# Kernel optimization log

Measured on AMD Instinct MI355X. Metric: run time of the kernel, lower is better.

Reference implementation:

```python
import jax, jax.numpy as jnp
import numpy as np

NUM_GROUP = 16
LN_EPS = 1e-5


def setup_inputs() -> dict:
    key = jax.random.key(0)
    ks = jax.random.split(key, 3)
    B, N, C = 8, 4096, 1024
    x = jax.random.normal(ks[0], (B, N, C), dtype=jnp.float32)
    Wqkv = jax.random.normal(ks[1], (C, 3 * C), dtype=jnp.float32) * (C ** -0.5)
    Wproj = jax.random.normal(ks[2], (C, C), dtype=jnp.float32) * (C ** -0.5)
    bproj = jnp.zeros((C,), dtype=jnp.float32)
    gamma = jnp.ones((C,), dtype=jnp.float32)
    beta = jnp.zeros((C,), dtype=jnp.float32)
    return {"x": x, "Wqkv": Wqkv, "Wproj": Wproj, "bproj": bproj,
            "gamma": gamma, "beta": beta}


def reference(x, Wqkv, Wproj, bproj, gamma, beta):
    B, N, C = x.shape
    G = NUM_GROUP
    hd = C // G
    scale = hd ** -0.5
    # QKV projection: [B,N,3,G,hd]
    qkv = (x @ Wqkv).reshape(B, N, 3, G, hd)
    q = jnp.transpose(qkv[:, :, 0], (0, 2, 1, 3))  # [B,G,N,hd]
    k = jnp.transpose(qkv[:, :, 1], (0, 2, 1, 3)) * scale
    v = jnp.transpose(qkv[:, :, 2], (0, 2, 1, 3))
    # transposed (channel) attention: k^T @ v -> [B,G,hd,hd]
    attn = jnp.einsum('bgnd,bgne->bgde', k, v)
    attn = jax.nn.softmax(attn, axis=-1)
    # (attn @ q^T)^T : out[b,g,n,d] = sum_e attn[b,g,d,e] * q[b,g,n,e]
    out = jnp.einsum('bgde,bgne->bgnd', attn, q)  # [B,G,N,hd]
    out = jnp.transpose(out, (0, 2, 1, 3)).reshape(B, N, C)
    out = out @ Wproj + bproj  # dropout is identity in eval mode
    h = x + out
    # LayerNorm over last dim
    mu = jnp.mean(h, axis=-1, keepdims=True)
    var = jnp.var(h, axis=-1, keepdims=True)
    return gamma * (h - mu) * jax.lax.rsqrt(var + LN_EPS) + beta
```

## Files before the change

### kernel.cpp

```cpp
#include <hip/hip_runtime.h>
#include <cstdint>

typedef __bf16 bf16;
typedef __bf16 bf16x8 __attribute__((ext_vector_type(8)));
typedef float f32x4 __attribute__((ext_vector_type(4)));

#define DEVI __device__ __forceinline__

DEVI float bits2f(uint32_t u){ union{uint32_t u;float f;}x; x.u=u; return x.f; }
DEVI uint32_t packbf2(float a, float b){
  union{ bf16 h[2]; uint32_t u; } p; p.h[0]=(bf16)a; p.h[1]=(bf16)b; return p.u;
}

DEVI void gload_lds16(const void* g, void* l){
  __builtin_amdgcn_global_load_lds(
    (const __attribute__((address_space(1))) uint32_t*)g,
    (__attribute__((address_space(3))) uint32_t*)l, 16, 0, 0);
}

__global__ __launch_bounds__(256) void k_cast(const float* __restrict__ x, bf16* __restrict__ o, int n){
  int i = (blockIdx.x*256 + threadIdx.x)*8;
  if (i >= n) return;
  float4 a = *(const float4*)(x+i);
  float4 b = *(const float4*)(x+i+4);
  union { bf16 h[8]; uint4 u; } r;
  r.h[0]=(bf16)a.x; r.h[1]=(bf16)a.y; r.h[2]=(bf16)a.z; r.h[3]=(bf16)a.w;
  r.h[4]=(bf16)b.x; r.h[5]=(bf16)b.y; r.h[6]=(bf16)b.z; r.h[7]=(bf16)b.w;
  *(uint4*)(o+i) = r.u;
}

__global__ __launch_bounds__(256) void k_castT(const float* __restrict__ x, bf16* __restrict__ xb,
                                               bf16* __restrict__ xT){
  const int b = blockIdx.z;
  x  += (size_t)b*4194304; xb += (size_t)b*4194304; xT += (size_t)b*4194304;
  const int n0 = blockIdx.y*64, c0 = blockIdx.x*64;
  __shared__ float sF[64][65];
  const int t = threadIdx.x;
  const int lr = t>>4, lc4 = (t&15)*4;
  #pragma unroll
  for (int i=0;i<4;++i){
    int r = lr + i*16;
    float4 v = *(const float4*)(x + (size_t)(n0+r)*1024 + c0 + lc4);
    sF[r][lc4+0]=v.x; sF[r][lc4+1]=v.y; sF[r][lc4+2]=v.z; sF[r][lc4+3]=v.w;
  }
  __syncthreads();
  const int wr = t>>3, wc8 = (t&7)*8;
  #pragma unroll
  for (int i=0;i<2;++i){
    int r = wr + i*32;
    union{ bf16 h[8]; uint4 u; } p;
    #pragma unroll
    for (int j=0;j<8;++j) p.h[j] = (bf16)sF[r][wc8+j];
    *(uint4*)(xb + (size_t)(n0+r)*1024 + c0 + wc8) = p.u;
  }
  #pragma unroll
  for (int i=0;i<2;++i){
    int c = wr + i*32;
    union{ bf16 h[8]; uint4 u; } p;
    #pragma unroll
    for (int j=0;j<8;++j) p.h[j] = (bf16)sF[wc8+j][c];
    *(uint4*)(xT + (size_t)(c0+c)*4096 + n0 + wc8) = p.u;
  }
}

__global__ __launch_bounds__(256) void k_transpose(const float* __restrict__ W, bf16* __restrict__ WT,
                                                   int R, int Ccols){
  __shared__ float tile[32][33];
  int bc = blockIdx.x*32, br = blockIdx.y*32;
  int lc = threadIdx.x & 31, lr = threadIdx.x >> 5;
  #pragma unroll
  for (int i=0;i<4;i++){
    int r = lr + i*8;
    tile[r][lc] = W[(size_t)(br+r)*Ccols + bc + lc];
  }
  __syncthreads();
  #pragma unroll
  for (int i=0;i<4;i++){
    int r = lr + i*8;
    WT[(size_t)(bc+r)*R + br + lc] = (bf16)tile[lc][r];
  }
}

__global__ __launch_bounds__(256) void k_gemm128(
    const bf16* __restrict__ A, const bf16* __restrict__ BT, bf16* __restrict__ C,
    int N, int K, int lda, int ldb,
    size_t As, size_t Bs, size_t Cs)
{
  A += blockIdx.z*As; BT += blockIdx.z*Bs; C += blockIdx.z*Cs;
  __shared__ __align__(16) bf16 sA[128*64];
  __shared__ __align__(16) bf16 sB[128*64];
  const int t = threadIdx.x, w = t>>6, l = t&63;
  const int bm = blockIdx.y*128, bn = blockIdx.x*128;
  const int wr = (w>>1)*64, wc = (w&1)*64;
  f32x4 acc[4][4] = {};
  const int srow = l>>3;
  const int scol = ((l&7) ^ (l>>3))*8;
  const int nk = K>>6;
  for (int kt=0; kt<nk; ++kt) {
    const int k0 = kt*64;
    #pragma unroll
    for (int i=0;i<4;++i){
      int c = w*4+i;
      int row = c*8 + srow;
      gload_lds16(A  + (size_t)(bm+row)*lda + k0 + scol, (char*)sA + c*1024);
      gload_lds16(BT + (size_t)(bn+row)*ldb + k0 + scol, (char*)sB + c*1024);
    }
    __syncthreads();
    #pragma unroll
    for (int kk=0; kk<64; kk+=32) {
      bf16x8 af[4], bfr[4];
      const int xr = ((kk + 8*(l>>4))*2) ^ ((l&7)<<4);
      #pragma unroll
      for (int mf=0;mf<4;++mf){
        int row = wr + mf*16 + (l&15);
        af[mf] = *(const bf16x8*)((const char*)sA + row*128 + xr);
      }
      #pragma unroll
      for (int nf=0;nf<4;++nf){
        int row = wc + nf*16 + (l&15);
        bfr[nf] = *(const bf16x8*)((const char*)sB + row*128 + xr);
      }
      #pragma unroll
      for (int mf=0;mf<4;++mf)
        #pragma unroll
        for (int nf=0;nf<4;++nf)
          acc[mf][nf] = __builtin_amdgcn_mfma_f32_16x16x32_bf16(af[mf], bfr[nf], acc[mf][nf], 0,0,0);
    }
    __syncthreads();
  }
  #pragma unroll
  for (int mf=0;mf<4;++mf)
    #pragma unroll
    for (int nf=0;nf<4;++nf)
      #pragma unroll
      for (int r=0;r<4;++r){
        int row = bm + wr + mf*16 + (l>>4)*4 + r;
        int col = bn + wc + nf*16 + (l&15);
        C[(size_t)row*N + col] = (bf16)acc[mf][nf][r];
      }
}

__global__ __launch_bounds__(256) void k_gramsym(const bf16* __restrict__ xT, bf16* __restrict__ Gram){
  const int d = blockIdx.y*36 + blockIdx.x;
  const int vt = (d & 7)*36 + (d >> 3);
  const int b = vt/36;
  int t36 = vt - b*36;
  int i = 0;
  while (t36 >= 8 - i){ t36 -= 8 - i; ++i; }
  const int j = i + t36;
  const bf16* A = xT + (size_t)b*4194304;
  bf16* C = Gram + (size_t)b*1048576;
  const int bm = i*128, bn = j*128;

  __shared__ __align__(16) bf16 sAB[16384];
  bf16* sA = sAB; bf16* sB = sAB + 8192;
  const int t = threadIdx.x, w = t>>6, l = t&63;
  const int wr = (w>>1)*64, wc = (w&1)*64;
  f32x4 acc[4][4] = {};
  const int srow = l>>3;
  const int scol = ((l&7) ^ (l>>3))*8;
  for (int kt=0; kt<64; ++kt) {
    const int k0 = kt*64;
    #pragma unroll
    for (int ii=0;ii<4;++ii){
      int c = w*4+ii;
      int row = c*8 + srow;
      gload_lds16(A + (size_t)(bm+row)*4096 + k0 + scol, (char*)sA + c*1024);
      gload_lds16(A + (size_t)(bn+row)*4096 + k0 + scol, (char*)sB + c*1024);
    }
    __syncthreads();
    #pragma unroll
    for (int kk=0; kk<64; kk+=32) {
      bf16x8 af[4], bfr[4];
      const int xr = ((kk + 8*(l>>4))*2) ^ ((l&7)<<4);
      #pragma unroll
      for (int mf=0;mf<4;++mf)
        af[mf] = *(const bf16x8*)((const char*)sA + (wr+mf*16+(l&15))*128 + xr);
      #pragma unroll
      for (int nf=0;nf<4;++nf)
        bfr[nf] = *(const bf16x8*)((const char*)sB + (wc+nf*16+(l&15))*128 + xr);
      #pragma unroll
      for (int mf=0;mf<4;++mf)
        #pragma unroll
        for (int nf=0;nf<4;++nf)
          acc[mf][nf] = __builtin_amdgcn_mfma_f32_16x16x32_bf16(af[mf], bfr[nf], acc[mf][nf], 0,0,0);
    }
    __syncthreads();
  }
  #pragma unroll
  for (int mf=0;mf<4;++mf)
    #pragma unroll
    for (int nf=0;nf<4;++nf)
      #pragma unroll
      for (int r=0;r<4;++r){
        int row = bm + wr + mf*16 + (l>>4)*4 + r;
        int col = bn + wc + nf*16 + (l&15);
        C[(size_t)row*1024 + col] = (bf16)acc[mf][nf][r];
      }
  if (i == j) return;
  for (int h2=0; h2<2; ++h2){
    __syncthreads();
    if ((w&1) == h2){
      #pragma unroll
      for (int mf=0;mf<4;++mf)
        #pragma unroll
        for (int nf=0;nf<4;++nf)
          #pragma unroll
          for (int p=0;p<2;++p){
            int col_local = nf*16 + (l&15);
            int rowb = wr + mf*16 + (l>>4)*4 + 2*p;
            *(uint32_t*)((char*)sAB + (col_local*136 + rowb)*2) =
              packbf2(acc[mf][nf][2*p], acc[mf][nf][2*p+1]);
          }
    }
    __syncthreads();
    {
      int col_local = t>>2, sub = t&3;
      const uint4* src = (const uint4*)((const char*)sAB + col_local*272 + sub*64);
      uint4 v0 = src[0], v1 = src[1], v2 = src[2], v3 = src[3];
      bf16* dst = C + (size_t)(bn + h2*64 + col_local)*1024 + bm + sub*32;
      ((uint4*)dst)[0]=v0; ((uint4*)dst)[1]=v1; ((uint4*)dst)[2]=v2; ((uint4*)dst)[3]=v3;
    }
  }
}

__global__ __launch_bounds__(512, 2) void k_gemm256(
    const bf16* __restrict__ A, const bf16* __restrict__ BT, bf16* __restrict__ C,
    int N, int K,
    const float* __restrict__ bias, const bf16* __restrict__ resid,
    size_t As, size_t Bs, size_t Cs, size_t Rs)
{
  A += blockIdx.z*As; BT += blockIdx.z*Bs; C += blockIdx.z*Cs; resid += blockIdx.z*Rs;
  __shared__ __align__(16) bf16 lds[2][2][256*64];
  bf16* bA0 = &lds[0][0][0]; bf16* bB0 = &lds[0][1][0];
  bf16* bA1 = &lds[1][0][0]; bf16* bB1 = &lds[1][1][0];

  const int t = threadIdx.x, w = t>>6, l = t&63;
  const int wm = w>>2, wn = w&3;

  const int nwg = gridDim.x * gridDim.y;
  const int orig = blockIdx.y * gridDim.x + blockIdx.x;
  const int q = nwg >> 3, r = nwg & 7;
  const int xcd = orig & 7, loc = orig >> 3;
  const int swz = (xcd < r ? xcd*(q+1) : r*(q+1) + (xcd-r)*q) + loc;
  const int bx = swz % gridDim.x, by = swz / gridDim.x;
  const int bm = by*256, bn = bx*256;

  const int co0 = (16*(l>>4)) ^ ((l&7)<<4);
  const int co1 = (64 + 16*(l>>4)) ^ ((l&7)<<4);

  auto stageA = [&](const bf16* G, bf16* Ldst, int j, int k0){
    int row = wm*128 + wn*32 + j*8 + (l>>3);
    int col = 8*((l&7) ^ (l>>3));
    gload_lds16(G + (size_t)(bm + row)*K + k0 + col,
                Ldst + (wm*128 + wn*32 + j*8)*64);
  };
  auto stageB = [&](const bf16* G, bf16* Ldst, int j, int k0){
    int row = j*64 + w*8 + (l>>3);
    int col = 8*((l&7) ^ (l>>3));
    gload_lds16(G + (size_t)(bn + row)*K + k0 + col,
                Ldst + (j*64 + w*8)*64);
  };

#define RD_AA(dst, qd, base) {                                                  \
    const int r0 = wm*128 + (qd)*32 + (l&15);                                   \
    dst[0][0] = *(const bf16x8*)((const char*)(base) + (r0   )*128 + co0);      \
    dst[0][1] = *(const bf16x8*)((const char*)(base) + (r0   )*128 + co1);      \
    dst[1][0] = *(const bf16x8*)((const char*)(base) + (r0+16)*128 + co0);      \
    dst[1][1] = *(const bf16x8*)((const char*)(base) + (r0+16)*128 + co1);      \
  }

#define MFMA_Q(P, AA) {                                                         \
    __builtin_amdgcn_s_setprio(1);                                              \
    _Pragma("unroll")                                                           \
    for (int kk=0;kk<2;++kk)                                                    \
      _Pragma("unroll")                                                         \
      for (int i=0;i<2;++i)                                                     \
        _Pragma("unroll")                                                       \
        for (int nf=0;nf<4;++nf)                                                \
          acc[2*(P)+i][nf] = __builtin_amdgcn_mfma_f32_16x16x32_bf16(           \
              AA[i][kk], bfr[nf][kk], acc[2*(P)+i][nf], 0,0,0);                 \
    __builtin_amdgcn_s_setprio(0);                                              \
  }

#define BAR asm volatile("s_barrier" ::: "memory")

  f32x4 acc[8][4] = {};
  const int NT = K >> 6;

  #pragma unroll
  for (int j=0;j<4;++j) stageA(A, bA0, j, 0);
  #pragma unroll
  for (int j=0;j<4;++j) stageB(BT, bB0, j, 0);
  __builtin_amdgcn_sched_barrier(0);
  if (NT > 1){
    #pragma unroll
    for (int j=0;j<4;++j) stageB(BT, bB1, j, 64);
    asm volatile("s_waitcnt vmcnt(4)" ::: "memory");
  } else {
    asm volatile("s_waitcnt vmcnt(0)" ::: "memory");
  }
  BAR;

  bf16x8 aaA[2][2], aaB[2][2];
  RD_AA(aaA, wn, bA0);

  for (int T = 0; T < NT; ++T){
    bf16* sA  = (T&1) ? bA1 : bA0;
    bf16* sB  = (T&1) ? bB1 : bB0;
    bf16* sAn = (T&1) ? bA0 : bA1;
    const int kA = (T+1)<<6, kB = (T+2)<<6;
    const bool stA = (T+1) < NT, stB = (T+2) < NT;

    bf16x8 bfr[4][2];
    const int rb = wn*64 + (l&15);
    #pragma unroll
    for (int nf=0;nf<4;++nf){
      bfr[nf][0] = *(const bf16x8*)((const char*)sB + (rb+nf*16)*128 + co0);
      bfr[nf][1] = *(const bf16x8*)((const char*)sB + (rb+nf*16)*128 + co1);
    }

    RD_AA(aaB, (wn+1)&3, sA);
    if (stA){ stageA(A, sAn, 0, kA); stageA(A, sAn, 1, kA); }
    BAR; MFMA_Q(0, aaA); BAR;

    RD_AA(aaA, (wn+2)&3, sA);
    if (stA){ stageA(A, sAn, 2, kA); stageA(A, sAn, 3, kA); }
    BAR; MFMA_Q(1, aaB); BAR;

    RD_AA(aaB, (wn+3)&3, sA);
    if (stB){ stageB(BT, sB, 0, kB); stageB(BT, sB, 1, kB); }
    BAR; MFMA_Q(2, aaA); BAR;

    if (stB){
      stageB(BT, sB, 2, kB); stageB(BT, sB, 3, kB);
      asm volatile("s_waitcnt vmcnt(4)" ::: "memory");
    } else {
      asm volatile("s_waitcnt vmcnt(0)" ::: "memory");
    }
    if (stA) RD_AA(aaA, wn, sAn);
    BAR; MFMA_Q(3, aaB); BAR;
  }
#undef RD_AA
#undef MFMA_Q
#undef BAR

  #pragma unroll
  for (int P=0; P<4; ++P){
    const int qd = (P+wn)&3;
    #pragma unroll
    for (int i=0;i<2;++i){
      #pragma unroll
      for (int nf=0; nf<4; ++nf){
        #pragma unroll
        for (int r2=0; r2<4; ++r2){
          int row = bm + wm*128 + qd*32 + i*16 + (l>>4)*4 + r2;
          int col = bn + wn*64 + nf*16 + (l&15);
          float v = acc[2*P+i][nf][r2] + bias[col] + (float)resid[(size_t)row*N + col];
          C[(size_t)row*N + col] = (bf16)v;
        }
      }
    }
  }
}

__global__ __launch_bounds__(256) void k_sgemm64(const bf16* __restrict__ T2, const bf16* __restrict__ WqkvT,
                                                 bf16* __restrict__ Aatt){
  const int bg = blockIdx.x, b = bg>>4, g = bg&15;
  const bf16* Arows = T2 + (size_t)b*1048576 + (size_t)(g*64)*1024;
  const bf16* Brows = WqkvT + (size_t)(2048 + g*64)*1024;
  __shared__ __align__(16) bf16 sA[64*64];
  __shared__ __align__(16) bf16 sB[64*64];
  const int t = threadIdx.x, w = t>>6, l = t&63;
  const int srow = l>>3, scol = ((l&7)^(l>>3))*8;
  f32x4 acc[4] = {};
  for (int kt=0; kt<16; ++kt){
    const int k0 = kt*64;
    gload_lds16(Arows + (size_t)(w*8+srow)*1024 + k0 + scol,      sA + (w*8)*64);
    gload_lds16(Arows + (size_t)(32+w*8+srow)*1024 + k0 + scol,   sA + (32+w*8)*64);
    gload_lds16(Brows + (size_t)(w*8+srow)*1024 + k0 + scol,      sB + (w*8)*64);
    gload_lds16(Brows + (size_t)(32+w*8+srow)*1024 + k0 + scol,   sB + (32+w*8)*64);
    __syncthreads();
    #pragma unroll
    for (int kk=0; kk<64; kk+=32){
      const int xr = ((kk + 8*(l>>4))*2) ^ ((l&7)<<4);
      bf16x8 af = *(const bf16x8*)((const char*)sA + (w*16+(l&15))*128 + xr);
      #pragma unroll
      for (int nf=0; nf<4; ++nf){
        bf16x8 bfv = *(const bf16x8*)((const char*)sB + (nf*16+(l&15))*128 + xr);
        acc[nf] = __builtin_amdgcn_mfma_f32_16x16x32_bf16(af, bfv, acc[nf], 0,0,0);
      }
    }
    __syncthreads();
  }
  #pragma unroll
  for (int reg=0; reg<4; ++reg){
    float m = -3.4e38f;
    #pragma unroll
    for (int nf=0; nf<4; ++nf) m = fmaxf(m, acc[nf][reg]);
    m = fmaxf(m, __shfl_xor(m,1)); m = fmaxf(m, __shfl_xor(m,2));
    m = fmaxf(m, __shfl_xor(m,4)); m = fmaxf(m, __shfl_xor(m,8));
    float e[4]; float s = 0.f;
    #pragma unroll
    for (int nf=0; nf<4; ++nf){ e[nf] = __expf((acc[nf][reg]-m)*0.125f); s += e[nf]; }
    s += __shfl_xor(s,1); s += __shfl_xor(s,2); s += __shfl_xor(s,4); s += __shfl_xor(s,8);
    const float inv = 1.0f/s;
    const int row = w*16 + (l>>4)*4 + reg;
    #pragma unroll
    for (int nf=0; nf<4; ++nf)
      Aatt[(size_t)bg*4096 + row*64 + nf*16 + (l&15)] = (bf16)(e[nf]*inv);
  }
}

__global__ __launch_bounds__(256) void k_applyW(const bf16* __restrict__ Wqkvb, const bf16* __restrict__ Aatt,
                                                bf16* __restrict__ U){
  const int bg = blockIdx.y, b = bg>>4, g = bg&15;
  const int m0 = blockIdx.x*128;
  __shared__ __align__(16) bf16 Pl[64][72];
  const int t = threadIdx.x, w = t>>6, l = t&63;
  for (int idx=t; idx<1024; idx+=256){
    int r2 = idx>>4, c4 = (idx&15)*4;
    *(uint2*)&Pl[r2][c4] = *(const uint2*)&Aatt[(size_t)bg*4096 + r2*64 + c4];
  }
  __syncthreads();
  f32x4 acc[2][4] = {};
  const bf16* Ab = Wqkvb + (size_t)(m0 + w*32)*3072 + g*64;
  #pragma unroll
  for (int kk=0; kk<64; kk+=32){
    bf16x8 af[2], pf[4];
    #pragma unroll
    for (int mf=0;mf<2;++mf)
      af[mf] = *(const bf16x8*)(Ab + (size_t)(mf*16 + (l&15))*3072 + kk + 8*(l>>4));
    #pragma unroll
    for (int nf=0;nf<4;++nf)
      pf[nf] = *(const bf16x8*)&Pl[nf*16 + (l&15)][kk + 8*(l>>4)];
    #pragma unroll
    for (int mf=0;mf<2;++mf)
      #pragma unroll
      for (int nf=0;nf<4;++nf)
        acc[mf][nf] = __builtin_amdgcn_mfma_f32_16x16x32_bf16(af[mf], pf[nf], acc[mf][nf], 0,0,0);
  }
  #pragma unroll
  for (int mf=0;mf<2;++mf)
    #pragma unroll
    for (int nf=0;nf<4;++nf)
      #pragma unroll
      for (int r=0;r<4;++r){
        int rowc = m0 + w*32 + mf*16 + (l>>4)*4 + r;
        int col = g*64 + nf*16 + (l&15);
        U[(size_t)b*1048576 + (size_t)rowc*1024 + col] = (bf16)acc[mf][nf][r];
      }
}

__global__ __launch_bounds__(256) void k_ln(const bf16* __restrict__ h, const float* __restrict__ gamma,
                                            const float* __restrict__ beta, float* __restrict__ y){
  const int w = threadIdx.x>>6, l = threadIdx.x&63;
  const size_t row = (size_t)blockIdx.x*4 + w;
  const bf16* hr = h + row*1024 + l*16;
  uint4 p0 = *(const uint4*)hr;
  uint4 p1 = *(const uint4*)(hr+8);
  float v[16];
  const uint32_t* pw = (const uint32_t*)&p0;
  #pragma unroll
  for (int i=0;i<4;++i){ v[2*i] = bits2f(pw[i]<<16); v[2*i+1] = bits2f(pw[i]&0xffff0000u); }
  const uint32_t* pw1 = (const uint32_t*)&p1;
  #pragma unroll
  for (int i=0;i<4;++i){ v[8+2*i] = bits2f(pw1[i]<<16); v[8+2*i+1] = bits2f(pw1[i]&0xffff0000u); }
  float s=0.f, s2=0.f;
  #pragma unroll
  for (int i=0;i<16;++i){ s+=v[i]; s2+=v[i]*v[i]; }
  #pragma unroll
  for (int off=1; off<64; off<<=1){ s += __shfl_xor(s,off); s2 += __shfl_xor(s2,off); }
  float mu = s*(1.0f/1024.0f);
  float var = s2*(1.0f/1024.0f) - mu*mu;
  float rinv = rsqrtf(var + 1e-5f);
  const float* gp = gamma + l*16; const float* bp = beta + l*16;
  float o[16];
  #pragma unroll
  for (int i=0;i<16;++i) o[i] = gp[i]*(v[i]-mu)*rinv + bp[i];
  float* yr = y + row*1024 + l*16;
  #pragma unroll
  for (int i=0;i<4;++i) ((float4*)yr)[i] = *(float4*)&o[4*i];
}

extern "C" void kernel_launch(void* const* d_in, const int* in_sizes, int n_in,
                              void* d_out, int out_size, void* d_ws, size_t ws_size,
                              hipStream_t stream){
  const float* x     = (const float*)d_in[0];
  const float* Wqkv  = (const float*)d_in[1];
  const float* Wproj = (const float*)d_in[2];
  const float* bproj = (const float*)d_in[3];
  const float* gamma = (const float*)d_in[4];
  const float* beta  = (const float*)d_in[5];
  float* y = (float*)d_out;

  char* ws = (char*)d_ws;
  size_t off = 0;
  auto alloc = [&](size_t bytes)->void*{ void* p = ws + off; off += (bytes + 255) & ~(size_t)255; return p; };
  bf16* xb     = (bf16*)alloc((size_t)32768*1024*2);
  bf16* xT     = (bf16*)alloc((size_t)8*1024*4096*2);
  bf16* Wqkvb  = (bf16*)alloc((size_t)1024*3072*2);
  bf16* WqkvT  = (bf16*)alloc((size_t)3072*1024*2);
  bf16* WprojT = (bf16*)alloc((size_t)1024*1024*2);
  bf16* Gram   = (bf16*)alloc((size_t)8*1024*1024*2);
  bf16* T2     = (bf16*)alloc((size_t)8*1024*1024*2);
  bf16* Aatt   = (bf16*)alloc((size_t)128*64*64*2);
  bf16* U      = (bf16*)alloc((size_t)8*1024*1024*2);
  bf16* WeffT  = (bf16*)alloc((size_t)8*1024*1024*2);
  bf16* h      = xT;

  const size_t MB1 = 1048576;

  k_castT<<<dim3(16,64,8),256,0,stream>>>(x, xb, xT);
  k_cast<<<1536,256,0,stream>>>(Wqkv, Wqkvb, 3145728);
  k_transpose<<<dim3(96,32),256,0,stream>>>(Wqkv, WqkvT, 1024, 3072);
  k_transpose<<<dim3(32,32),256,0,stream>>>(Wproj, WprojT, 1024, 1024);
  k_gramsym<<<dim3(36,8),256,0,stream>>>(xT, Gram);
  k_gemm128<<<dim3(8,8,8),256,0,stream>>>(WqkvT + (size_t)1024*1024, Gram, T2, 1024, 1024, 1024, 1024,
                                          0, MB1, MB1);
  k_sgemm64<<<128,256,0,stream>>>(T2, WqkvT, Aatt);
  k_applyW<<<dim3(8,128),256,0,stream>>>(Wqkvb, Aatt, U);
  k_gemm128<<<dim3(8,8,8),256,0,stream>>>(WprojT, U, WeffT, 1024, 1024, 1024, 1024,
                                          0, MB1, MB1);
  k_gemm256<<<dim3(4,16,8),512,0,stream>>>(xb, WeffT, h, 1024, 1024, bproj, xb,
                                           (size_t)4096*1024, MB1, (size_t)4096*1024, (size_t)4096*1024);
  k_ln<<<8192,256,0,stream>>>(h, gamma, beta, y);
}
```

Measured before the change: 333.4 us.

## Split Gram GEMM over K into two partial blocks plus reduce kernel

The symmetric Gram kernel is split along the K dimension into two halves, doubling the grid from 288 to 576 blocks. Each block writes an fp32 partial tile, and a new reduce kernel sums the two partials, casts to bf16 and writes both the tile and its mirrored transpose. The aim is better occupancy of the GPU's CUs, since 288 blocks underfill the device. The cost is an extra kernel launch and about 38 MB of fp32 partial-tile traffic written and read back.

```diff
diff --git a/kernel.cpp b/kernel.cpp
--- a/kernel.cpp
+++ b/kernel.cpp
@@ -8,9 +8,6 @@
 #define DEVI __device__ __forceinline__
 
 DEVI float bits2f(uint32_t u){ union{uint32_t u;float f;}x; x.u=u; return x.f; }
-DEVI uint32_t packbf2(float a, float b){
-  union{ bf16 h[2]; uint32_t u; } p; p.h[0]=(bf16)a; p.h[1]=(bf16)b; return p.u;
-}
 
 DEVI void gload_lds16(const void* g, void* l){
   __builtin_amdgcn_global_load_lds(
@@ -140,27 +137,31 @@
       }
 }
 
-__global__ __launch_bounds__(256) void k_gramsym(const bf16* __restrict__ xT, bf16* __restrict__ Gram){
-  const int d = blockIdx.y*36 + blockIdx.x;
-  const int vt = (d & 7)*36 + (d >> 3);
-  const int b = vt/36;
-  int t36 = vt - b*36;
+__global__ __launch_bounds__(256) void k_gramsplit(const bf16* __restrict__ xT, float* __restrict__ Gp){
+  const int d = blockIdx.z*288 + blockIdx.y*36 + blockIdx.x;
+  const int vt = (d & 7)*72 + (d >> 3);
+  const int b = vt/72;
+  const int rem = vt - b*72;
+  const int half = rem >= 36 ? 1 : 0;
+  const int t36o = rem - 36*half;
+  int t36 = t36o;
   int i = 0;
   while (t36 >= 8 - i){ t36 -= 8 - i; ++i; }
   const int j = i + t36;
   const bf16* A = xT + (size_t)b*4194304;
-  bf16* C = Gram + (size_t)b*1048576;
+  float* P = Gp + ((size_t)((half*8 + b)*36 + t36o))*16384;
   const int bm = i*128, bn = j*128;
-
-  __shared__ __align__(16) bf16 sAB[16384];
-  bf16* sA = sAB; bf16* sB = sAB + 8192;
+  const int kbase = half*2048;
+
+  __shared__ __align__(16) bf16 sA[128*64];
+  __shared__ __align__(16) bf16 sB[128*64];
   const int t = threadIdx.x, w = t>>6, l = t&63;
   const int wr = (w>>1)*64, wc = (w&1)*64;
   f32x4 acc[4][4] = {};
   const int srow = l>>3;
   const int scol = ((l&7) ^ (l>>3))*8;
-  for (int kt=0; kt<64; ++kt) {
-    const int k0 = kt*64;
+  for (int kt=0; kt<32; ++kt) {
+    const int k0 = kbase + kt*64;
     #pragma unroll
     for (int ii=0;ii<4;++ii){
       int c = w*4+ii;
@@ -192,35 +193,50 @@
     #pragma unroll
     for (int nf=0;nf<4;++nf)
       #pragma unroll
-      for (int r=0;r<4;++r){
-        int row = bm + wr + mf*16 + (l>>4)*4 + r;
-        int col = bn + wc + nf*16 + (l&15);
-        C[(size_t)row*1024 + col] = (bf16)acc[mf][nf][r];
-      }
+      for (int r=0;r<4;++r)
+        P[(wr + mf*16 + (l>>4)*4 + r)*128 + wc + nf*16 + (l&15)] = acc[mf][nf][r];
+}
+
+__global__ __launch_bounds__(256) void k_gramreduce(const float* __restrict__ Gp, bf16* __restrict__ Gram){
+  const int b = blockIdx.y;
+  const int t36o = blockIdx.x;
+  int t36 = t36o;
+  int i = 0;
+  while (t36 >= 8 - i){ t36 -= 8 - i; ++i; }
+  const int j = i + t36;
+  const float* P0 = Gp + ((size_t)(b*36) + t36o)*16384;
+  const float* P1 = Gp + ((size_t)((8+b)*36) + t36o)*16384;
+  bf16* C = Gram + (size_t)b*1048576;
+  const int bm = i*128, bn = j*128;
+  __shared__ float sT[128][129];
+  const int t = threadIdx.x;
+  const int rr = t>>4, cc = (t&15)*8;
+  #pragma unroll
+  for (int ch=0; ch<8; ++ch){
+    const int row = ch*16 + rr;
+    const int idx = row*128 + cc;
+    float4 a0 = *(const float4*)(P0+idx), a1 = *(const float4*)(P0+idx+4);
+    float4 b0 = *(const float4*)(P1+idx), b1 = *(const float4*)(P1+idx+4);
+    float s[8] = {a0.x+b0.x, a0.y+b0.y, a0.z+b0.z, a0.w+b0.w,
+                  a1.x+b1.x, a1.y+b1.y, a1.z+b1.z, a1.w+b1.w};
+    union{ bf16 h[8]; uint4 u; } p;
+    #pragma unroll
+    for (int k=0;k<8;++k) p.h[k] = (bf16)s[k];
+    *(uint4*)(C + (size_t)(bm+row)*1024 + bn + cc) = p.u;
+    if (i != j){
+      #pragma unroll
+      for (int k=0;k<8;++k) sT[row][cc+k] = s[k];
+    }
+  }
   if (i == j) return;
-  for (int h2=0; h2<2; ++h2){
-    __syncthreads();
-    if ((w&1) == h2){
-      #pragma unroll
-      for (int mf=0;mf<4;++mf)
-        #pragma unroll
-        for (int nf=0;nf<4;++nf)
-          #pragma unroll
-          for (int p=0;p<2;++p){
-            int col_local = nf*16 + (l&15);
-            int rowb = wr + mf*16 + (l>>4)*4 + 2*p;
-            *(uint32_t*)((char*)sAB + (col_local*136 + rowb)*2) =
-              packbf2(acc[mf][nf][2*p], acc[mf][nf][2*p+1]);
-          }
-    }
-    __syncthreads();
-    {
-      int col_local = t>>2, sub = t&3;
-      const uint4* src = (const uint4*)((const char*)sAB + col_local*272 + sub*64);
-      uint4 v0 = src[0], v1 = src[1], v2 = src[2], v3 = src[3];
-      bf16* dst = C + (size_t)(bn + h2*64 + col_local)*1024 + bm + sub*32;
-      ((uint4*)dst)[0]=v0; ((uint4*)dst)[1]=v1; ((uint4*)dst)[2]=v2; ((uint4*)dst)[3]=v3;
-    }
+  __syncthreads();
+  #pragma unroll
+  for (int ch=0; ch<8; ++ch){
+    const int c = ch*16 + rr;
+    union{ bf16 h[8]; uint4 u; } p;
+    #pragma unroll
+    for (int k=0;k<8;++k) p.h[k] = (bf16)sT[cc+k][c];
+    *(uint4*)(C + (size_t)(bn+c)*1024 + bm + cc) = p.u;
   }
 }
 
@@ -497,17 +513,18 @@
   char* ws = (char*)d_ws;
   size_t off = 0;
   auto alloc = [&](size_t bytes)->void*{ void* p = ws + off; off += (bytes + 255) & ~(size_t)255; return p; };
-  bf16* xb     = (bf16*)alloc((size_t)32768*1024*2);
-  bf16* xT     = (bf16*)alloc((size_t)8*1024*4096*2);
-  bf16* Wqkvb  = (bf16*)alloc((size_t)1024*3072*2);
-  bf16* WqkvT  = (bf16*)alloc((size_t)3072*1024*2);
-  bf16* WprojT = (bf16*)alloc((size_t)1024*1024*2);
-  bf16* Gram   = (bf16*)alloc((size_t)8*1024*1024*2);
-  bf16* T2     = (bf16*)alloc((size_t)8*1024*1024*2);
-  bf16* Aatt   = (bf16*)alloc((size_t)128*64*64*2);
-  bf16* U      = (bf16*)alloc((size_t)8*1024*1024*2);
-  bf16* WeffT  = (bf16*)alloc((size_t)8*1024*1024*2);
-  bf16* h      = xT;
+  bf16*  xb     = (bf16*) alloc((size_t)32768*1024*2);
+  bf16*  xT     = (bf16*) alloc((size_t)8*1024*4096*2);
+  bf16*  Wqkvb  = (bf16*) alloc((size_t)1024*3072*2);
+  bf16*  WqkvT  = (bf16*) alloc((size_t)3072*1024*2);
+  bf16*  WprojT = (bf16*) alloc((size_t)1024*1024*2);
+  bf16*  Gram   = (bf16*) alloc((size_t)8*1024*1024*2);
+  bf16*  T2     = (bf16*) alloc((size_t)8*1024*1024*2);
+  bf16*  Aatt   = (bf16*) alloc((size_t)128*64*64*2);
+  bf16*  U      = (bf16*) alloc((size_t)8*1024*1024*2);
+  bf16*  WeffT  = (bf16*) alloc((size_t)8*1024*1024*2);
+  float* Gpart  = (float*)alloc((size_t)2*8*36*16384*4);
+  bf16*  h      = xT;
 
   const size_t MB1 = 1048576;
 
@@ -515,7 +532,8 @@
   k_cast<<<1536,256,0,stream>>>(Wqkv, Wqkvb, 3145728);
   k_transpose<<<dim3(96,32),256,0,stream>>>(Wqkv, WqkvT, 1024, 3072);
   k_transpose<<<dim3(32,32),256,0,stream>>>(Wproj, WprojT, 1024, 1024);
-  k_gramsym<<<dim3(36,8),256,0,stream>>>(xT, Gram);
+  k_gramsplit<<<dim3(36,8,2),256,0,stream>>>(xT, Gpart);
+  k_gramreduce<<<dim3(36,8),256,0,stream>>>(Gpart, Gram);
   k_gemm128<<<dim3(8,8,8),256,0,stream>>>(WqkvT + (size_t)1024*1024, Gram, T2, 1024, 1024, 1024, 1024,
                                           0, MB1, MB1);
   k_sgemm64<<<128,256,0,stream>>>(T2, WqkvT, Aatt);
```

After: 350.2 us. 1.05x slower.
